# Kernel tuning notes

Hardware: AMD Instinct MI355X
Metric: run time of the kernel (lower is better)

The kernel has to match this reference:

```python
import jax, jax.numpy as jnp
import numpy as np

VOCAB = 32000; PAD = 0
NHID = 512; H = 8; NK = 64; NV = 64; NL = 4
B = 16; S = 511; L = S + 1
N = B * S            # graph nodes after reshape(-1, n_hid)
E = 131072           # edges per graph
EPS = 1e-5
PATTERN = [0, 0, 1, 1, 0, 0, 1, 1]  # n_head==8 -> [gt,gt,attr,attr,gt,gt,attr,attr]


def setup_inputs() -> dict:
    key = jax.random.key(0)
    ks = iter(jax.random.split(key, 48))
    r = lambda *sh: jax.random.normal(next(ks), sh, jnp.float32) * 0.02
    inp = {}
    emb = jax.random.normal(next(ks), (VOCAB, NHID), jnp.float32) * 0.1
    inp['in_embed_w'] = emb.at[PAD].set(0.0)            # padding_idx row is zero
    inp['pos_embed_w'] = jax.random.normal(next(ks), (L, NHID), jnp.float32) * 0.1
    inp['qkv_w'] = r(NL, NHID, H * (2 * NK + NV)); inp['qkv_b'] = r(NL, H * (2 * NK + NV))
    inp['attn_out_w'] = r(NL, H * NV, NHID); inp['attn_out_b'] = r(NL, NHID)
    inp['ff1_w'] = r(NL, NHID, 4 * NHID); inp['ff1_b'] = r(NL, 4 * NHID)
    inp['ff2_w'] = r(NL, 4 * NHID, NHID); inp['ff2_b'] = r(NL, NHID)
    inp['sage1_w'] = r(H, NHID, NHID); inp['sage1_b'] = r(H, NHID)
    inp['sage2_w'] = r(H, NHID, NHID); inp['sage2_b'] = r(H, NHID)
    inp['gc3_w'] = r(H, NHID, NHID // H); inp['gc3_b'] = r(H, NHID // H)
    inp['gcn_ff1_w'] = r(NHID, NHID); inp['gcn_ff1_b'] = r(NHID)
    inp['gcn_ff2_w'] = r(NHID, NHID); inp['gcn_ff2_b'] = r(NHID)
    inp['ln_g'] = jnp.ones((NHID,), jnp.float32)
    inp['ln_b'] = jnp.zeros((NHID,), jnp.float32)
    inp['in_idxs'] = jax.random.randint(next(ks), (B, S), 1, VOCAB)
    inp['mask'] = jnp.ones((B, L, H, L), dtype=bool)
    inp['gt_src'] = jax.random.randint(next(ks), (E,), 0, N)
    inp['gt_dst'] = jax.random.randint(next(ks), (E,), 0, N)
    inp['attr_src'] = jax.random.randint(next(ks), (E,), 0, N)
    inp['attr_dst'] = jax.random.randint(next(ks), (E,), 0, N)
    return inp


def _ln(x, g, b):
    mu = x.mean(-1, keepdims=True)
    v = ((x - mu) ** 2).mean(-1, keepdims=True)
    return (x - mu) / jnp.sqrt(v + EPS) * g + b


def _encode(in_embed_w, pos_embed_w, qkv_w, qkv_b, attn_out_w, attn_out_b,
            ff1_w, ff1_b, ff2_w, ff2_b, sage1_w, sage1_b, sage2_w, sage2_b,
            gc3_w, gc3_b, gcn_ff1_w, gcn_ff1_b, gcn_ff2_w, gcn_ff2_b, ln_g, ln_b,
            in_idxs, mask, gt_src, gt_dst, attr_src, attr_dst):
    # --- embed (pad one pad-token column at the front) ---
    pad_idxs = jnp.pad(in_idxs, ((0, 0), (1, 0)), constant_values=PAD)
    h = in_embed_w[pad_idxs] + pos_embed_w[jnp.arange(L)]        # [B,L,NHID]
    m = mask.transpose(0, 2, 1, 3)                               # [B,H,L,L]
    # --- transformer blocks ---
    for l in range(NL):
        qkv = (h @ qkv_w[l] + qkv_b[l]).reshape(B, L, H, 2 * NK + NV).transpose(0, 2, 1, 3)
        q, k, v = qkv[..., :NK], qkv[..., NK:2 * NK], qkv[..., 2 * NK:]
        sc = jnp.einsum('bhik,bhjk->bhij', q, k) / np.float32(np.sqrt(NK))
        sc = jnp.where(m, sc, -jnp.inf)
        a = jax.nn.softmax(sc, axis=-1)
        o = jnp.einsum('bhij,bhjd->bhid', a, v).transpose(0, 2, 1, 3).reshape(B, L, H * NV)
        attn_ret = h + (o @ attn_out_w[l] + attn_out_b[l])       # attn module returns x + out
        x = h + attn_ret                                         # block adds x again (faithful)
        h = x + (jax.nn.relu(x @ ff1_w[l] + ff1_b[l]) @ ff2_w[l] + ff2_b[l])
    zg, hg = h[:, 0], h[:, 1:]                                   # [B,NHID], [B,S,NHID]
    # --- GCN over flattened nodes ---
    xf = hg.reshape(N, NHID)
    def deg(idx):
        return jax.ops.segment_sum(jnp.ones((E,), jnp.float32), idx, num_segments=N)
    gdata = []
    for src, dst in ((gt_src, gt_dst), (attr_src, attr_dst)):
        gdata.append((src, dst, deg(dst), deg(src)))             # (src, dst, in_deg, out_deg)
    outs = []
    for i in range(H):
        src, dst, ind, outd = gdata[PATTERN[i]]
        def sage(x, W, b):
            # DGL SAGEConv 'gcn': (sum_neigh + self) / (in_deg + 1) then linear
            agg = jax.ops.segment_sum(x[src], dst, num_segments=N)
            return ((agg + x) / (ind + 1.0)[:, None]) @ W + b
        o = sage(xf, sage1_w[i], sage1_b[i])
        o = sage(o, sage2_w[i], sage2_b[i])
        # DGL GraphConv norm='both' (in>out so weight first)
        f = (o @ gc3_w[i]) * (jnp.maximum(outd, 1.0) ** -0.5)[:, None]
        agg = jax.ops.segment_sum(f[src], dst, num_segments=N)
        outs.append(agg * (jnp.maximum(ind, 1.0) ** -0.5)[:, None] + gc3_b[i])
    xc = jnp.concatenate(outs, axis=-1).reshape(B, S, NHID)
    x = hg + _ln(xc, ln_g, ln_b)
    ff = jax.nn.relu(x @ gcn_ff1_w + gcn_ff1_b) @ gcn_ff2_w + gcn_ff2_b
    zbar = x + _ln(ff, ln_g, ln_b)
    return zbar, zg


def reference(in_embed_w, pos_embed_w, qkv_w, qkv_b, attn_out_w, attn_out_b,
              ff1_w, ff1_b, ff2_w, ff2_b, sage1_w, sage1_b, sage2_w, sage2_b,
              gc3_w, gc3_b, gcn_ff1_w, gcn_ff1_b, gcn_ff2_w, gcn_ff2_b, ln_g, ln_b,
              in_idxs, mask, gt_src, gt_dst, attr_src, attr_dst):
    return _encode(in_embed_w, pos_embed_w, qkv_w, qkv_b, attn_out_w, attn_out_b,
                   ff1_w, ff1_b, ff2_w, ff2_b, sage1_w, sage1_b, sage2_w, sage2_b,
                   gc3_w, gc3_b, gcn_ff1_w, gcn_ff1_b, gcn_ff2_w, gcn_ff2_b, ln_g, ln_b,
                   in_idxs, mask, gt_src, gt_dst, attr_src, attr_dst)
```

## Files before the change

### kernel.cpp

```cpp
#include <hip/hip_runtime.h>
#include <hip/hip_bf16.h>

typedef __hip_bfloat16 bf16;
typedef unsigned short u16;
typedef __attribute__((ext_vector_type(8))) short s16x8;
typedef __attribute__((ext_vector_type(4))) float f32x4;

__device__ __forceinline__ float bfb(unsigned short b) {
    union { unsigned u; float f; } v; v.u = ((unsigned)b) << 16; return v.f;
}
__device__ __forceinline__ float ldin(const void* p, size_t i, bool f32) {
    return f32 ? ((const float*)p)[i] : bfb(((const unsigned short*)p)[i]);
}
__device__ __forceinline__ void ld4(const void* p, size_t i, bool f32,
                                    float& x, float& y, float& z, float& w) {
    if (f32) {
        float4 v = *reinterpret_cast<const float4*>((const float*)p + i);
        x = v.x; y = v.y; z = v.z; w = v.w;
    } else {
        ushort4 u = *reinterpret_cast<const ushort4*>((const unsigned short*)p + i);
        x = bfb(u.x); y = bfb(u.y); z = bfb(u.z); w = bfb(u.w);
    }
}
__device__ __forceinline__ u16 f2b(float x) {
    bf16 h = __float2bfloat16(x);
    return *reinterpret_cast<u16*>(&h);
}
__device__ __forceinline__ void split2(float x, u16& h, u16& l) {
    unsigned u = __float_as_uint(x);
    h = (u16)(u >> 16);
    float rem = x - __uint_as_float(u & 0xFFFF0000u);
    l = f2b(rem);
}
__device__ __forceinline__ int xcd_swz(int F, int nwg) {
    return ((nwg & 7) == 0) ? ((F & 7) * (nwg >> 3) + (F >> 3)) : F;
}

constexpr int C_B = 16, C_S = 511, C_L = 512, C_NHID = 512;
constexpr int C_N = C_B * C_S;
constexpr int C_MTOK = C_B * C_L;
constexpr int C_E = 131072;
constexpr int C_QKVD = 1536;

enum : size_t {
    OFF_H     = 0,
    OFF_QKV   = 4194304,
    OFF_O     = 16777216,
    OFF_X     = 20971520,
    OFF_MID   = 25165824,
    OFF_PRE   = 41943040,
    OFF_T8    = OFF_PRE,
    OFF_GCAT0 = OFF_PRE + 262144,
    OFF_GCAT1 = OFF_GCAT0 + 131072,
    OFF_DCAT0 = OFF_GCAT1 + 131072,
    OFF_DCAT1 = OFF_DCAT0 + 256,
    OFF_DEG   = OFF_DCAT1 + 256,
    OFF_FLAG  = OFF_DEG + 32768
};

__global__ void detect_kernel(const unsigned* __restrict__ g, int* __restrict__ flag) {
    *flag = (g[0] == 0x3F800000u) ? 1 : 0;
}

__global__ __launch_bounds__(256) void embed_kernel(
    const void* __restrict__ emb, const void* __restrict__ pos,
    const int* __restrict__ idxs, const int* __restrict__ flag,
    float* __restrict__ h)
{
    const bool f = (*flag) != 0;
    int token = blockIdx.x;
    int tid = threadIdx.x;
    int b = token >> 9, t = token & 511;
    int id = (t == 0) ? 0 : idxs[b * C_S + t - 1];
    size_t eo = (size_t)id * C_NHID, po = (size_t)t * C_NHID, ho = (size_t)token * C_NHID;
    h[ho + tid]       = ldin(emb, eo + tid, f)       + ldin(pos, po + tid, f);
    h[ho + tid + 256] = ldin(emb, eo + tid + 256, f) + ldin(pos, po + tid + 256, f);
}

__global__ __launch_bounds__(256) void wtrans2_kernel(
    const void* __restrict__ Wsrc, size_t srcOff, const int* __restrict__ flag,
    u16* __restrict__ Bh, u16* __restrict__ Bl, int K, int N)
{
    const bool f = (*flag) != 0;
    __shared__ float s[32][33];
    int nb = blockIdx.x << 5, kb = blockIdx.y << 5;
    int c = threadIdx.x & 31, r0 = (threadIdx.x >> 5) << 2;
#pragma unroll
    for (int i = 0; i < 4; ++i)
        s[r0 + i][c] = ldin(Wsrc, srcOff + (size_t)(kb + r0 + i) * N + nb + c, f);
    __syncthreads();
#pragma unroll
    for (int i = 0; i < 4; ++i) {
        u16 h, l;
        split2(s[c][r0 + i], h, l);
        size_t o = (size_t)(nb + r0 + i) * K + kb + c;
        Bh[o] = h; Bl[o] = l;
    }
}

__global__ __launch_bounds__(256, 2) void msgemm_kernel(
    const float* __restrict__ A,
    const u16* __restrict__ Bh, const u16* __restrict__ Bl,
    const void* __restrict__ biasB, size_t bOff,
    const float* __restrict__ biasF,
    const float* __restrict__ res, float resScale,
    const float* __restrict__ rowDeg, int relu,
    const int* __restrict__ flag,
    float* __restrict__ C, int M, int K, int Nc, int ldc)
{
    const bool f32in = (*flag) != 0;
    __shared__ __align__(16) u16 sAh[128][40];
    __shared__ __align__(16) u16 sAl[128][40];
    __shared__ __align__(16) u16 sBh[64][40];
    __shared__ __align__(16) u16 sBl[64][40];
    const int tid = threadIdx.x;
    const int nwg = gridDim.x * gridDim.y;
    const int swz = xcd_swz(blockIdx.y * gridDim.x + blockIdx.x, nwg);
    const int bm = (swz / gridDim.x) << 7, bn = (swz % gridDim.x) << 6;
    const int lane = tid & 63, lr = lane & 15, lg = lane >> 4;
    const int wave = tid >> 6, wm = wave >> 1, wn = wave & 1;

    f32x4 acc[4][2];
#pragma unroll
    for (int m = 0; m < 4; ++m)
#pragma unroll
        for (int n = 0; n < 2; ++n) {
            f32x4 z = {0.f, 0.f, 0.f, 0.f};
            acc[m][n] = z;
        }

    const int sr = tid >> 1, sk = (tid & 1) << 4;
    const int am = bm + sr;
    const bool aok = am < M;
    const float* ap = A + (size_t)am * K + sk;
    const int brn = tid >> 2, bk = (tid & 3) << 3;
    const u16* bph = Bh + (size_t)(bn + brn) * K + bk;
    const u16* bpl = Bl + (size_t)(bn + brn) * K + bk;

    for (int k0 = 0; k0 < K; k0 += 32) {
        u16 tah[16], tal[16];
        if (aok) {
#pragma unroll
            for (int i = 0; i < 16; i += 4) {
                float4 v = *reinterpret_cast<const float4*>(ap + k0 + i);
                split2(v.x, tah[i],     tal[i]);
                split2(v.y, tah[i + 1], tal[i + 1]);
                split2(v.z, tah[i + 2], tal[i + 2]);
                split2(v.w, tah[i + 3], tal[i + 3]);
            }
        } else {
#pragma unroll
            for (int i = 0; i < 16; ++i) { tah[i] = 0; tal[i] = 0; }
        }
        s16x8 bh0 = *reinterpret_cast<const s16x8*>(bph + k0);
        s16x8 bl0 = *reinterpret_cast<const s16x8*>(bpl + k0);

        *reinterpret_cast<s16x8*>(&sAh[sr][sk])     = *reinterpret_cast<s16x8*>(&tah[0]);
        *reinterpret_cast<s16x8*>(&sAh[sr][sk + 8]) = *reinterpret_cast<s16x8*>(&tah[8]);
        *reinterpret_cast<s16x8*>(&sAl[sr][sk])     = *reinterpret_cast<s16x8*>(&tal[0]);
        *reinterpret_cast<s16x8*>(&sAl[sr][sk + 8]) = *reinterpret_cast<s16x8*>(&tal[8]);
        *reinterpret_cast<s16x8*>(&sBh[brn][bk]) = bh0;
        *reinterpret_cast<s16x8*>(&sBl[brn][bk]) = bl0;
        __syncthreads();

        s16x8 fah[4], fal[4], fbh[2], fbl[2];
#pragma unroll
        for (int m = 0; m < 4; ++m) {
            fah[m] = *reinterpret_cast<const s16x8*>(&sAh[wm * 64 + m * 16 + lr][lg * 8]);
            fal[m] = *reinterpret_cast<const s16x8*>(&sAl[wm * 64 + m * 16 + lr][lg * 8]);
        }
#pragma unroll
        for (int n = 0; n < 2; ++n) {
            fbh[n] = *reinterpret_cast<const s16x8*>(&sBh[wn * 32 + n * 16 + lr][lg * 8]);
            fbl[n] = *reinterpret_cast<const s16x8*>(&sBl[wn * 32 + n * 16 + lr][lg * 8]);
        }
#pragma unroll
        for (int m = 0; m < 4; ++m)
#pragma unroll
            for (int n = 0; n < 2; ++n) {
                acc[m][n] = __builtin_amdgcn_mfma_f32_16x16x32_bf16(fah[m], fbh[n], acc[m][n], 0, 0, 0);
                acc[m][n] = __builtin_amdgcn_mfma_f32_16x16x32_bf16(fah[m], fbl[n], acc[m][n], 0, 0, 0);
                acc[m][n] = __builtin_amdgcn_mfma_f32_16x16x32_bf16(fal[m], fbh[n], acc[m][n], 0, 0, 0);
            }
        __syncthreads();
    }

#pragma unroll
    for (int m = 0; m < 4; ++m) {
#pragma unroll
        for (int r = 0; r < 4; ++r) {
            int row = bm + wm * 64 + m * 16 + lg * 4 + r;
            if (row >= M) continue;
            float rs = rowDeg ? rsqrtf(fmaxf(rowDeg[row], 1.f)) : 1.f;
#pragma unroll
            for (int n = 0; n < 2; ++n) {
                int col = bn + wn * 32 + n * 16 + lr;
                float v = acc[m][n][r];
                if (biasB) v += ldin(biasB, bOff + col, f32in);
                if (biasF) v += biasF[col];
                v *= rs;
                if (res) v += resScale * res[(size_t)row * Nc + col];
                if (relu) v = fmaxf(v, 0.f);
                C[(size_t)row * ldc + col] = v;
            }
        }
    }
}

__global__ __launch_bounds__(256, 2) void msgemm2_kernel(
    const float* __restrict__ A,
    const u16* __restrict__ Bh, const u16* __restrict__ Bl,
    const void* __restrict__ biasB, size_t bOff,
    const int relu, const int* __restrict__ flag,
    float* __restrict__ C, int M, int K, int Nc, int ldc)
{
    const bool f32in = (*flag) != 0;
    __shared__ __align__(16) u16 sAh[128][40];
    __shared__ __align__(16) u16 sAl[128][40];
    __shared__ __align__(16) u16 sBh[128][40];
    __shared__ __align__(16) u16 sBl[128][40];
    const int tid = threadIdx.x;
    const int nwg = gridDim.x * gridDim.y;
    const int swz = xcd_swz(blockIdx.y * gridDim.x + blockIdx.x, nwg);
    const int bm = (swz / gridDim.x) << 7, bn = (swz % gridDim.x) << 7;
    const int lane = tid & 63, lr = lane & 15, lg = lane >> 4;
    const int wave = tid >> 6, wm = wave >> 1, wn = wave & 1;

    f32x4 acc[4][4];
#pragma unroll
    for (int m = 0; m < 4; ++m)
#pragma unroll
        for (int n = 0; n < 4; ++n) {
            f32x4 z = {0.f, 0.f, 0.f, 0.f};
            acc[m][n] = z;
        }

    const int sr = tid >> 1, sk = (tid & 1) << 4;
    const int am = bm + sr;
    const bool aok = am < M;
    const float* ap = A + (size_t)am * K + sk;
    const u16* bph = Bh + (size_t)(bn + sr) * K + sk;
    const u16* bpl = Bl + (size_t)(bn + sr) * K + sk;

    for (int k0 = 0; k0 < K; k0 += 32) {
        u16 tah[16], tal[16];
        if (aok) {
#pragma unroll
            for (int i = 0; i < 16; i += 4) {
                float4 v = *reinterpret_cast<const float4*>(ap + k0 + i);
                split2(v.x, tah[i],     tal[i]);
                split2(v.y, tah[i + 1], tal[i + 1]);
                split2(v.z, tah[i + 2], tal[i + 2]);
                split2(v.w, tah[i + 3], tal[i + 3]);
            }
        } else {
#pragma unroll
            for (int i = 0; i < 16; ++i) { tah[i] = 0; tal[i] = 0; }
        }
        s16x8 bh0 = *reinterpret_cast<const s16x8*>(bph + k0);
        s16x8 bh1 = *reinterpret_cast<const s16x8*>(bph + k0 + 8);
        s16x8 bl0 = *reinterpret_cast<const s16x8*>(bpl + k0);
        s16x8 bl1 = *reinterpret_cast<const s16x8*>(bpl + k0 + 8);

        *reinterpret_cast<s16x8*>(&sAh[sr][sk])     = *reinterpret_cast<s16x8*>(&tah[0]);
        *reinterpret_cast<s16x8*>(&sAh[sr][sk + 8]) = *reinterpret_cast<s16x8*>(&tah[8]);
        *reinterpret_cast<s16x8*>(&sAl[sr][sk])     = *reinterpret_cast<s16x8*>(&tal[0]);
        *reinterpret_cast<s16x8*>(&sAl[sr][sk + 8]) = *reinterpret_cast<s16x8*>(&tal[8]);
        *reinterpret_cast<s16x8*>(&sBh[sr][sk])     = bh0;
        *reinterpret_cast<s16x8*>(&sBh[sr][sk + 8]) = bh1;
        *reinterpret_cast<s16x8*>(&sBl[sr][sk])     = bl0;
        *reinterpret_cast<s16x8*>(&sBl[sr][sk + 8]) = bl1;
        __syncthreads();

        s16x8 fah[4], fal[4], fbh[4], fbl[4];
#pragma unroll
        for (int m = 0; m < 4; ++m) {
            fah[m] = *reinterpret_cast<const s16x8*>(&sAh[wm * 64 + m * 16 + lr][lg * 8]);
            fal[m] = *reinterpret_cast<const s16x8*>(&sAl[wm * 64 + m * 16 + lr][lg * 8]);
        }
#pragma unroll
        for (int n = 0; n < 4; ++n) {
            fbh[n] = *reinterpret_cast<const s16x8*>(&sBh[wn * 64 + n * 16 + lr][lg * 8]);
            fbl[n] = *reinterpret_cast<const s16x8*>(&sBl[wn * 64 + n * 16 + lr][lg * 8]);
        }
#pragma unroll
        for (int m = 0; m < 4; ++m)
#pragma unroll
            for (int n = 0; n < 4; ++n) {
                acc[m][n] = __builtin_amdgcn_mfma_f32_16x16x32_bf16(fah[m], fbh[n], acc[m][n], 0, 0, 0);
                acc[m][n] = __builtin_amdgcn_mfma_f32_16x16x32_bf16(fah[m], fbl[n], acc[m][n], 0, 0, 0);
                acc[m][n] = __builtin_amdgcn_mfma_f32_16x16x32_bf16(fal[m], fbh[n], acc[m][n], 0, 0, 0);
            }
        __syncthreads();
    }

#pragma unroll
    for (int m = 0; m < 4; ++m) {
#pragma unroll
        for (int r = 0; r < 4; ++r) {
            int row = bm + wm * 64 + m * 16 + lg * 4 + r;
            if (row >= M) continue;
#pragma unroll
            for (int n = 0; n < 4; ++n) {
                int col = bn + wn * 64 + n * 16 + lr;
                float v = acc[m][n][r];
                if (biasB) v += ldin(biasB, bOff + col, f32in);
                if (relu) v = fmaxf(v, 0.f);
                C[(size_t)row * ldc + col] = v;
            }
        }
    }
}

__global__ __launch_bounds__(256) void mattn_kernel(
    const float* __restrict__ qkv, float* __restrict__ o_out)
{
    __shared__ __align__(16) u16 sKh[64][72], sKl[64][72];
    __shared__ __align__(16) u16 sVh[64][72], sVl[64][72];
    __shared__ __align__(16) u16 sPh[4][16][72], sPl[4][16][72];
    const int blk = xcd_swz(blockIdx.x, gridDim.x);
    const int b = blk >> 6, h = (blk >> 3) & 7, qt = blk & 7;
    const int tid = threadIdx.x;
    const int lane = tid & 63, lr = lane & 15, lg = lane >> 4;
    const int w = tid >> 6;

    s16x8 qh[2], ql[2];
    {
        const float* qp = qkv + (size_t)(b * C_L + qt * 64 + w * 16 + lr) * C_QKVD + h * 192;
#pragma unroll
        for (int c = 0; c < 2; ++c) {
            int d0 = c * 32 + lg * 8;
            u16 th[8], tl[8];
#pragma unroll
            for (int i = 0; i < 8; i += 4) {
                float4 v = *reinterpret_cast<const float4*>(qp + d0 + i);
                split2(v.x * 0.125f, th[i],     tl[i]);
                split2(v.y * 0.125f, th[i + 1], tl[i + 1]);
                split2(v.z * 0.125f, th[i + 2], tl[i + 2]);
                split2(v.w * 0.125f, th[i + 3], tl[i + 3]);
            }
            qh[c] = *reinterpret_cast<s16x8*>(th);
            ql[c] = *reinterpret_cast<s16x8*>(tl);
        }
    }

    f32x4 accO[4];
#pragma unroll
    for (int n = 0; n < 4; ++n) { f32x4 z = {0.f, 0.f, 0.f, 0.f}; accO[n] = z; }
    float m[4] = {-3.0e38f, -3.0e38f, -3.0e38f, -3.0e38f};
    float l[4] = {0.f, 0.f, 0.f, 0.f};

    const float* kvb = qkv + (size_t)b * C_L * C_QKVD + h * 192;
    const int kp = tid >> 2;
    const int d0 = (tid & 3) << 4;

    for (int jt = 0; jt < 8; ++jt) {
        __syncthreads();
        {
            const float* kr = kvb + (size_t)(jt * 64 + kp) * C_QKVD + 64 + d0;
            const float* vr = kr + 64;
#pragma unroll
            for (int i = 0; i < 16; i += 4) {
                float4 kv = *reinterpret_cast<const float4*>(kr + i);
                float4 vv = *reinterpret_cast<const float4*>(vr + i);
                u16 th[4], tl[4];
                split2(kv.x, th[0], tl[0]); split2(kv.y, th[1], tl[1]);
                split2(kv.z, th[2], tl[2]); split2(kv.w, th[3], tl[3]);
                *reinterpret_cast<ushort4*>(&sKh[kp][d0 + i]) = *reinterpret_cast<ushort4*>(th);
                *reinterpret_cast<ushort4*>(&sKl[kp][d0 + i]) = *reinterpret_cast<ushort4*>(tl);
                u16 hh, ll;
                split2(vv.x, hh, ll); sVh[d0 + i][kp]     = hh; sVl[d0 + i][kp]     = ll;
                split2(vv.y, hh, ll); sVh[d0 + i + 1][kp] = hh; sVl[d0 + i + 1][kp] = ll;
                split2(vv.z, hh, ll); sVh[d0 + i + 2][kp] = hh; sVl[d0 + i + 2][kp] = ll;
                split2(vv.w, hh, ll); sVh[d0 + i + 3][kp] = hh; sVl[d0 + i + 3][kp] = ll;
            }
        }
        __syncthreads();

        f32x4 accS[4];
#pragma unroll
        for (int n = 0; n < 4; ++n) { f32x4 z = {0.f, 0.f, 0.f, 0.f}; accS[n] = z; }
#pragma unroll
        for (int n = 0; n < 4; ++n)
#pragma unroll
            for (int c = 0; c < 2; ++c) {
                s16x8 kh = *reinterpret_cast<const s16x8*>(&sKh[n * 16 + lr][c * 32 + lg * 8]);
                s16x8 kl = *reinterpret_cast<const s16x8*>(&sKl[n * 16 + lr][c * 32 + lg * 8]);
                accS[n] = __builtin_amdgcn_mfma_f32_16x16x32_bf16(qh[c], kh, accS[n], 0, 0, 0);
                accS[n] = __builtin_amdgcn_mfma_f32_16x16x32_bf16(qh[c], kl, accS[n], 0, 0, 0);
                accS[n] = __builtin_amdgcn_mfma_f32_16x16x32_bf16(ql[c], kh, accS[n], 0, 0, 0);
            }

#pragma unroll
        for (int r = 0; r < 4; ++r) {
            float mt = fmaxf(fmaxf(accS[0][r], accS[1][r]), fmaxf(accS[2][r], accS[3][r]));
            mt = fmaxf(mt, __shfl_xor(mt, 1));
            mt = fmaxf(mt, __shfl_xor(mt, 2));
            mt = fmaxf(mt, __shfl_xor(mt, 4));
            mt = fmaxf(mt, __shfl_xor(mt, 8));
            float mn = fmaxf(m[r], mt);
            float corr = __expf(m[r] - mn);
            m[r] = mn;
            float ps = 0.f;
#pragma unroll
            for (int n = 0; n < 4; ++n) {
                float p = __expf(accS[n][r] - mn);
                accS[n][r] = p;
                ps += p;
            }
            ps += __shfl_xor(ps, 1);
            ps += __shfl_xor(ps, 2);
            ps += __shfl_xor(ps, 4);
            ps += __shfl_xor(ps, 8);
            l[r] = l[r] * corr + ps;
#pragma unroll
            for (int n2 = 0; n2 < 4; ++n2) accO[n2][r] *= corr;
        }

#pragma unroll
        for (int r = 0; r < 4; ++r)
#pragma unroll
            for (int n = 0; n < 4; ++n) {
                u16 hh, ll;
                split2(accS[n][r], hh, ll);
                sPh[w][lg * 4 + r][n * 16 + lr] = hh;
                sPl[w][lg * 4 + r][n * 16 + lr] = ll;
            }
        __syncthreads();

#pragma unroll
        for (int n2 = 0; n2 < 4; ++n2)
#pragma unroll
            for (int c = 0; c < 2; ++c) {
                s16x8 ph = *reinterpret_cast<const s16x8*>(&sPh[w][lr][c * 32 + lg * 8]);
                s16x8 pl = *reinterpret_cast<const s16x8*>(&sPl[w][lr][c * 32 + lg * 8]);
                s16x8 vh = *reinterpret_cast<const s16x8*>(&sVh[n2 * 16 + lr][c * 32 + lg * 8]);
                s16x8 vl = *reinterpret_cast<const s16x8*>(&sVl[n2 * 16 + lr][c * 32 + lg * 8]);
                accO[n2] = __builtin_amdgcn_mfma_f32_16x16x32_bf16(ph, vh, accO[n2], 0, 0, 0);
                accO[n2] = __builtin_amdgcn_mfma_f32_16x16x32_bf16(ph, vl, accO[n2], 0, 0, 0);
                accO[n2] = __builtin_amdgcn_mfma_f32_16x16x32_bf16(pl, vh, accO[n2], 0, 0, 0);
            }
    }

#pragma unroll
    for (int r = 0; r < 4; ++r) {
        float inv = 1.f / l[r];
        float* op = o_out + (size_t)(b * C_L + qt * 64 + w * 16 + lg * 4 + r) * C_NHID + h * 64;
#pragma unroll
        for (int n2 = 0; n2 < 4; ++n2)
            op[n2 * 16 + lr] = accO[n2][r] * inv;
    }
}

__global__ __launch_bounds__(256) void sgemm64b_kernel(
    const void* __restrict__ A, int aIn, size_t aOff, size_t zA,
    const void* __restrict__ Wt, int wIn, size_t wOff, size_t zW,
    const int* __restrict__ flag,
    float* __restrict__ C, size_t zC, int M, int K, int Nc)
{
    const bool f32in = (*flag) != 0;
    const bool aF32 = aIn ? f32in : true;
    const bool wF32 = wIn ? f32in : true;
    const size_t za = aOff + (size_t)blockIdx.z * zA;
    const size_t zw = wOff + (size_t)blockIdx.z * zW;
    float* Cz = C + (size_t)blockIdx.z * zC;

    __shared__ float sA[16][68];
    __shared__ float sB[16][68];
    const int tid = threadIdx.x;
    const int tx = tid & 15, ty = tid >> 4;
    const int bm = blockIdx.y << 6, bn = blockIdx.x << 6;
    float acc[4][4] = {};
    const int la_r = tid >> 2;
    const int la_c = (tid & 3) << 2;
    const int lb_r = tid >> 4;
    const int lb_c = (tid & 15) << 2;

    for (int k0 = 0; k0 < K; k0 += 16) {
        float a0, a1, a2, a3, b0, b1, b2, b3;
        ld4(A, za + (size_t)(bm + la_r) * K + k0 + la_c, aF32, a0, a1, a2, a3);
        ld4(Wt, zw + (size_t)(k0 + lb_r) * Nc + bn + lb_c, wF32, b0, b1, b2, b3);
        sA[la_c + 0][la_r] = a0; sA[la_c + 1][la_r] = a1;
        sA[la_c + 2][la_r] = a2; sA[la_c + 3][la_r] = a3;
        sB[lb_r][lb_c + 0] = b0; sB[lb_r][lb_c + 1] = b1;
        sB[lb_r][lb_c + 2] = b2; sB[lb_r][lb_c + 3] = b3;
        __syncthreads();
#pragma unroll
        for (int kk = 0; kk < 16; ++kk) {
            float av[4], bv[4];
#pragma unroll
            for (int i = 0; i < 4; ++i) av[i] = sA[kk][(ty << 2) + i];
#pragma unroll
            for (int j = 0; j < 4; ++j) bv[j] = sB[kk][(tx << 2) + j];
#pragma unroll
            for (int i = 0; i < 4; ++i)
#pragma unroll
                for (int j = 0; j < 4; ++j)
                    acc[i][j] += av[i] * bv[j];
        }
        __syncthreads();
    }
#pragma unroll
    for (int i = 0; i < 4; ++i)
#pragma unroll
        for (int j = 0; j < 4; ++j)
            Cz[(size_t)(bm + (ty << 2) + i) * Nc + bn + (tx << 2) + j] = acc[i][j];
}

__global__ __launch_bounds__(256) void gcatT2_kernel(
    const float* __restrict__ Gtmp,
    u16* __restrict__ G0h, u16* __restrict__ G0l,
    u16* __restrict__ G1h, u16* __restrict__ G1l)
{
    int idx = blockIdx.x * 256 + threadIdx.x;
    int i = idx >> 15, rem = idx & 32767;
    int k = rem >> 6, c = rem & 63;
    int g = (i >> 1) & 1;
    int slot = (i & 1) + ((i >> 2) << 1);
    u16 h, l;
    split2(Gtmp[idx], h, l);
    size_t o = (size_t)(slot * 64 + c) * 512 + k;
    if (g) { G1h[o] = h; G1l[o] = l; }
    else   { G0h[o] = h; G0l[o] = l; }
}

__global__ __launch_bounds__(256) void xfcopy_kernel(
    const float* __restrict__ h, float* __restrict__ xf)
{
    int idx = blockIdx.x * 256 + threadIdx.x;
    int n = idx >> 9, c = idx & 511;
    int b = n / C_S;
    int s = n - b * C_S;
    xf[idx] = h[(((size_t)(b * C_L + 1 + s)) << 9) + c];
}

__global__ __launch_bounds__(256) void degi_kernel(
    const int* __restrict__ gs, const int* __restrict__ gd,
    const int* __restrict__ as_, const int* __restrict__ ad,
    int* __restrict__ ideg0, int* __restrict__ ideg1,
    float* __restrict__ outd0, float* __restrict__ outd1)
{
    int e = blockIdx.x * 256 + threadIdx.x;
    if (e >= C_E) return;
    atomicAdd(&ideg0[gd[e]], 1);
    atomicAdd(&ideg1[ad[e]], 1);
    atomicAdd(&outd0[gs[e]], 1.f);
    atomicAdd(&outd1[as_[e]], 1.f);
}

__global__ __launch_bounds__(1024) void scan_kernel(
    const int* __restrict__ i0, const int* __restrict__ i1,
    int* __restrict__ r0, int* __restrict__ r1)
{
    __shared__ int part[1024];
    const int t = threadIdx.x;
    const int* d = blockIdx.x ? i1 : i0;
    int* rs = blockIdx.x ? r1 : r0;
    int v[8]; int s = 0;
#pragma unroll
    for (int i = 0; i < 8; ++i) {
        int idx = t * 8 + i;
        v[i] = (idx < C_N) ? d[idx] : 0;
        s += v[i];
    }
    part[t] = s;
    __syncthreads();
    for (int off = 1; off < 1024; off <<= 1) {
        int x = (t >= off) ? part[t - off] : 0;
        __syncthreads();
        part[t] += x;
        __syncthreads();
    }
    int run = part[t] - s;
#pragma unroll
    for (int i = 0; i < 8; ++i) {
        int idx = t * 8 + i;
        if (idx <= C_N) rs[idx] = run;
        run += v[i];
    }
}

__global__ __launch_bounds__(256) void fill_kernel(
    const int* __restrict__ gs, const int* __restrict__ gd,
    const int* __restrict__ as_, const int* __restrict__ ad,
    const int* __restrict__ rs0, const int* __restrict__ rs1,
    int* __restrict__ cur0, int* __restrict__ cur1,
    int* __restrict__ csr0, int* __restrict__ csr1)
{
    int e = blockIdx.x * 256 + threadIdx.x;
    if (e >= C_E) return;
    int d0 = gd[e];
    int p = atomicAdd(&cur0[d0], 1);
    csr0[rs0[d0] + p] = gs[e];
    int d1 = ad[e];
    int q = atomicAdd(&cur1[d1], 1);
    csr1[rs1[d1] + q] = as_[e];
}

__global__ __launch_bounds__(256) void gatherA_kernel(
    const float* __restrict__ X, const int* __restrict__ csr,
    const int* __restrict__ rs, float* __restrict__ Y)
{
    const int n = blockIdx.x;
    const int tid = threadIdx.x;
    const int s0 = rs[n], s1 = rs[n + 1];
    const size_t o = (size_t)n * 512;
    float a0 = X[o + tid], a1 = X[o + tid + 256];
    for (int e = s0; e < s1; ++e) {
        const size_t so = (size_t)csr[e] * 512;
        a0 += X[so + tid];
        a1 += X[so + tid + 256];
    }
    const float r = 1.f / (float)(s1 - s0 + 1);
    Y[o + tid] = a0 * r;
    Y[o + tid + 256] = a1 * r;
}

__global__ __launch_bounds__(256) void gatherF_kernel(
    const float* __restrict__ F, const int* __restrict__ csr,
    const int* __restrict__ rs, float* __restrict__ xcagg,
    int c0, int c1, int c2, int c3)
{
    const int n = blockIdx.x;
    const int c = threadIdx.x;
    const int s0 = rs[n], s1 = rs[n + 1];
    float acc = 0.f;
    for (int e = s0; e < s1; ++e)
        acc += F[(size_t)csr[e] * 256 + c];
    const int s = c >> 6, cc = c & 63;
    const int cmap = (s == 0) ? c0 : (s == 1) ? c1 : (s == 2) ? c2 : c3;
    xcagg[(size_t)n * 512 + cmap + cc] = acc;
}

__global__ __launch_bounds__(256) void fxc_kernel(
    float* __restrict__ xcagg, const int* __restrict__ rs0,
    const int* __restrict__ rs1, const void* __restrict__ g3b,
    const int* __restrict__ flag)
{
    const bool f = (*flag) != 0;
    unsigned idx = blockIdx.x * 256 + threadIdx.x;
    int n = idx >> 7;
    int c = (idx & 127) << 2;
    int hh = c >> 6;
    int g = (hh >> 1) & 1;
    const int* rs = g ? rs1 : rs0;
    float ind = (float)(rs[n + 1] - rs[n]);
    float r = rsqrtf(fmaxf(ind, 1.f));
    size_t o = (size_t)n * 512 + c;
    float4 v = *reinterpret_cast<float4*>(xcagg + o);
    v.x = v.x * r + ldin(g3b, c, f);     v.y = v.y * r + ldin(g3b, c + 1, f);
    v.z = v.z * r + ldin(g3b, c + 2, f); v.w = v.w * r + ldin(g3b, c + 3, f);
    *reinterpret_cast<float4*>(xcagg + o) = v;
}

__global__ __launch_bounds__(512) void dvec_kernel(
    const void* __restrict__ s1b, const void* __restrict__ s2b,
    const void* __restrict__ g3w, const float* __restrict__ T8,
    const int* __restrict__ flag, float* __restrict__ dc0, float* __restrict__ dc1)
{
    const bool f = (*flag) != 0;
    const int i = blockIdx.x;
    const int c = threadIdx.x & 63;
    const int kg = threadIdx.x >> 6;
    const float* T = T8 + (size_t)i * 32768;
    float acc = 0.f;
    const int kbeg = kg * 64, kend = kbeg + 64;
    for (int k = kbeg; k < kend; ++k)
        acc += ldin(s1b, (size_t)i * 512 + k, f) * T[k * 64 + c]
             + ldin(s2b, (size_t)i * 512 + k, f) * ldin(g3w, (size_t)i * 32768 + (size_t)k * 64 + c, f);
    __shared__ float red[8][64];
    red[kg][c] = acc;
    __syncthreads();
    if (kg == 0) {
        float v = red[0][c] + red[1][c] + red[2][c] + red[3][c]
                + red[4][c] + red[5][c] + red[6][c] + red[7][c];
        int g = (i >> 1) & 1;
        int slot = (i & 1) + ((i >> 2) << 1);
        (g ? dc1 : dc0)[slot * 64 + c] = v;
    }
}

__global__ __launch_bounds__(256) void ln_kernel(
    const float* __restrict__ in, const float* __restrict__ res,
    const void* __restrict__ gw, const void* __restrict__ bw,
    const int* __restrict__ flag, float* __restrict__ out)
{
    const bool f = (*flag) != 0;
    int row = blockIdx.x;
    int tid = threadIdx.x;
    const float* x = in + (size_t)row * 512;
    float v0 = x[tid], v1 = x[tid + 256];
    __shared__ float red[4];
    float s = v0 + v1;
#pragma unroll
    for (int off = 32; off > 0; off >>= 1) s += __shfl_down(s, off);
    if ((tid & 63) == 0) red[tid >> 6] = s;
    __syncthreads();
    float mu = (red[0] + red[1] + red[2] + red[3]) * (1.f / 512.f);
    __syncthreads();
    float d0 = v0 - mu, d1 = v1 - mu;
    s = d0 * d0 + d1 * d1;
#pragma unroll
    for (int off = 32; off > 0; off >>= 1) s += __shfl_down(s, off);
    if ((tid & 63) == 0) red[tid >> 6] = s;
    __syncthreads();
    float var = (red[0] + red[1] + red[2] + red[3]) * (1.f / 512.f);
    float rstd = rsqrtf(var + 1e-5f);
    size_t o = (size_t)row * 512;
    float r0 = d0 * rstd * ldin(gw, tid, f)       + ldin(bw, tid, f);
    float r1 = d1 * rstd * ldin(gw, tid + 256, f) + ldin(bw, tid + 256, f);
    if (res) { r0 += res[o + tid]; r1 += res[o + tid + 256]; }
    out[o + tid] = r0;
    out[o + tid + 256] = r1;
}

__global__ __launch_bounds__(256) void out_zbar_kernel(
    const float* __restrict__ z, void* __restrict__ out, const int* __restrict__ flag)
{
    const bool f = (*flag) != 0;
    int idx = blockIdx.x * 256 + threadIdx.x;
    if (f) ((float*)out)[idx] = z[idx];
    else   ((bf16*)out)[idx]  = __float2bfloat16(z[idx]);
}

__global__ __launch_bounds__(256) void out_zg_kernel(
    const float* __restrict__ h, void* __restrict__ out, const int* __restrict__ flag)
{
    const bool f = (*flag) != 0;
    int idx = blockIdx.x * 256 + threadIdx.x;
    int b = idx >> 9, c = idx & 511;
    float v = h[(size_t)b * C_L * 512 + c];
    size_t o = (size_t)C_N * 512 + idx;
    if (f) ((float*)out)[o] = v;
    else   ((bf16*)out)[o]  = __float2bfloat16(v);
}

static inline void msgemm(hipStream_t st,
    const float* A, const u16* Bh, const u16* Bl,
    const void* biasB, size_t bOff, const float* biasF,
    const float* res, float resScale, const float* rowDeg, int relu,
    const int* flag, float* C, int M, int K, int Nc, int ldc)
{
    dim3 g(Nc / 64, (M + 127) / 128);
    msgemm_kernel<<<g, dim3(256), 0, st>>>(A, Bh, Bl, biasB, bOff, biasF,
                                           res, resScale, rowDeg, relu, flag,
                                           C, M, K, Nc, ldc);
}

static inline void msgemm2(hipStream_t st,
    const float* A, const u16* Bh, const u16* Bl,
    const void* biasB, size_t bOff, int relu,
    const int* flag, float* C, int M, int K, int Nc, int ldc)
{
    dim3 g(Nc / 128, (M + 127) / 128);
    msgemm2_kernel<<<g, dim3(256), 0, st>>>(A, Bh, Bl, biasB, bOff, relu, flag,
                                            C, M, K, Nc, ldc);
}

static inline void wtrans2(hipStream_t st, const void* Wsrc, size_t srcOff,
                           const int* flag, u16* Bh, u16* Bl, int K, int N)
{
    wtrans2_kernel<<<dim3(N / 32, K / 32), dim3(256), 0, st>>>(
        Wsrc, srcOff, flag, Bh, Bl, K, N);
}

extern "C" void kernel_launch(void* const* d_in, const int* in_sizes, int n_in,
                              void* d_out, int out_size, void* d_ws, size_t ws_size,
                              hipStream_t stream)
{
    const void* emb   = d_in[0];
    const void* pos   = d_in[1];
    const void* qkv_w = d_in[2];
    const void* qkv_b = d_in[3];
    const void* aow   = d_in[4];
    const void* aob   = d_in[5];
    const void* ff1w  = d_in[6];
    const void* ff1b  = d_in[7];
    const void* ff2w  = d_in[8];
    const void* ff2b  = d_in[9];
    const void* s1w   = d_in[10];
    const void* s1b   = d_in[11];
    const void* s2w   = d_in[12];
    const void* s2b   = d_in[13];
    const void* g3w   = d_in[14];
    const void* g3b   = d_in[15];
    const void* gf1w  = d_in[16];
    const void* gf1b  = d_in[17];
    const void* gf2w  = d_in[18];
    const void* gf2b  = d_in[19];
    const void* lng   = d_in[20];
    const void* lnb   = d_in[21];
    const int* idxs   = (const int*)d_in[22];
    const int* gts    = (const int*)d_in[24];
    const int* gtd    = (const int*)d_in[25];
    const int* ats    = (const int*)d_in[26];
    const int* atd    = (const int*)d_in[27];

    float* W = (float*)d_ws;
    float* h    = W + OFF_H;
    float* qkvb = W + OFF_QKV;
    float* ob   = W + OFF_O;
    float* xb   = W + OFF_X;
    float* midb = W + OFF_MID;
    int* flag   = (int*)(W + OFF_FLAG);

    detect_kernel<<<dim3(1), dim3(1), 0, stream>>>((const unsigned*)lng, flag);

    embed_kernel<<<dim3(C_MTOK), dim3(256), 0, stream>>>(emb, pos, idxs, flag, h);

    u16* qkvT = (u16*)ob;
    u16* aoT  = (u16*)midb;
    u16* ffT  = (u16*)qkvb;

    for (int l = 0; l < 4; ++l) {
        wtrans2(stream, qkv_w, (size_t)l * 512 * 1536, flag,
                qkvT, qkvT + 786432, 512, 1536);
        msgemm2(stream, h, qkvT, qkvT + 786432, qkv_b, (size_t)l * 1536,
                0, flag, qkvb, C_MTOK, 512, 1536, 1536);
        mattn_kernel<<<dim3(1024), dim3(256), 0, stream>>>(qkvb, ob);
        wtrans2(stream, aow, (size_t)l * 512 * 512, flag,
                aoT, aoT + 262144, 512, 512);
        msgemm(stream, ob, aoT, aoT + 262144, aob, (size_t)l * 512, nullptr,
               h, 2.f, nullptr, 0, flag, xb, C_MTOK, 512, 512, 512);
        wtrans2(stream, ff1w, (size_t)l * 512 * 2048, flag,
                ffT, ffT + 1048576, 512, 2048);
        msgemm2(stream, xb, ffT, ffT + 1048576, ff1b, (size_t)l * 2048,
                1, flag, midb, C_MTOK, 512, 2048, 2048);
        wtrans2(stream, ff2w, (size_t)l * 2048 * 512, flag,
                ffT + 2097152, ffT + 3145728, 2048, 512);
        msgemm(stream, midb, ffT + 2097152, ffT + 3145728, ff2b, (size_t)l * 512, nullptr,
               xb, 1.f, nullptr, 0, flag, h, C_MTOK, 2048, 512, 512);
    }

    float* xf    = ob;
    float* Z0    = qkvb;
    float* Z1    = qkvb + 4194304;
    float* Yb    = qkvb + 8388608;
    float* Gtmp  = Yb;
    float* Fb    = xb;
    float* zbar  = xb;
    float* xcagg = midb;
    float* xgnn  = midb + 4194304;
    float* fmid  = midb + 8388608;
    float* fout  = midb + 12582912;
    float* T8    = W + OFF_T8;
    float* dc0   = W + OFF_DCAT0;
    float* dc1   = W + OFF_DCAT1;
    float* outd0 = W + OFF_DEG;
    float* outd1 = outd0 + 8192;
    u16* GcT0h = (u16*)(W + OFF_GCAT0);
    u16* GcT0l = GcT0h + 131072;
    u16* GcT1h = (u16*)(W + OFF_GCAT1);
    u16* GcT1l = GcT1h + 131072;
    u16* gfT   = (u16*)Yb;

    int* ibase = (int*)fmid;
    int* rs0   = ibase;
    int* rs1   = ibase + 8208;
    int* ideg0 = ibase + 16416;
    int* ideg1 = ibase + 24608;
    int* cur0  = ibase + 32800;
    int* cur1  = ibase + 40992;
    int* csr0  = ibase + 49184;
    int* csr1  = ibase + 180256;

    xfcopy_kernel<<<dim3(C_N * 512 / 256), dim3(256), 0, stream>>>(h, xf);

    (void)hipMemsetAsync(ideg0, 0, 2 * 8192 * sizeof(int), stream);
    (void)hipMemsetAsync(cur0, 0, 2 * 8192 * sizeof(int), stream);
    (void)hipMemsetAsync(outd0, 0, 2 * 8192 * sizeof(float), stream);
    degi_kernel<<<dim3(C_E / 256), dim3(256), 0, stream>>>(
        gts, gtd, ats, atd, ideg0, ideg1, outd0, outd1);
    scan_kernel<<<dim3(2), dim3(1024), 0, stream>>>(ideg0, ideg1, rs0, rs1);
    fill_kernel<<<dim3(C_E / 256), dim3(256), 0, stream>>>(
        gts, gtd, ats, atd, rs0, rs1, cur0, cur1, csr0, csr1);

    sgemm64b_kernel<<<dim3(1, 8, 8), dim3(256), 0, stream>>>(
        s2w, 1, 0, 262144, g3w, 1, 0, 32768, flag, T8, 32768, 512, 512, 64);
    sgemm64b_kernel<<<dim3(1, 8, 8), dim3(256), 0, stream>>>(
        s1w, 1, 0, 262144, T8, 0, 0, 32768, flag, Gtmp, 32768, 512, 512, 64);
    gcatT2_kernel<<<dim3(1024), dim3(256), 0, stream>>>(Gtmp, GcT0h, GcT0l, GcT1h, GcT1l);
    dvec_kernel<<<dim3(8), dim3(512), 0, stream>>>(s1b, s2b, g3w, T8, flag, dc0, dc1);

    gatherA_kernel<<<dim3(C_N), dim3(256), 0, stream>>>(xf, csr0, rs0, Yb);
    gatherA_kernel<<<dim3(C_N), dim3(256), 0, stream>>>(Yb, csr0, rs0, Z0);
    gatherA_kernel<<<dim3(C_N), dim3(256), 0, stream>>>(xf, csr1, rs1, Yb);
    gatherA_kernel<<<dim3(C_N), dim3(256), 0, stream>>>(Yb, csr1, rs1, Z1);

    msgemm(stream, Z0, GcT0h, GcT0l, nullptr, 0, dc0, nullptr, 0.f, outd0, 0, flag,
           Fb, C_N, 512, 256, 256);
    gatherF_kernel<<<dim3(C_N), dim3(256), 0, stream>>>(
        Fb, csr0, rs0, xcagg, 0, 64, 256, 320);
    msgemm(stream, Z1, GcT1h, GcT1l, nullptr, 0, dc1, nullptr, 0.f, outd1, 0, flag,
           Fb, C_N, 512, 256, 256);
    gatherF_kernel<<<dim3(C_N), dim3(256), 0, stream>>>(
        Fb, csr1, rs1, xcagg, 128, 192, 384, 448);
    fxc_kernel<<<dim3(C_N * 128 / 256), dim3(256), 0, stream>>>(
        xcagg, rs0, rs1, g3b, flag);

    ln_kernel<<<dim3(C_N), dim3(256), 0, stream>>>(xcagg, xf, lng, lnb, flag, xgnn);
    wtrans2(stream, gf1w, 0, flag, gfT, gfT + 262144, 512, 512);
    msgemm(stream, xgnn, gfT, gfT + 262144, gf1b, 0, nullptr,
           nullptr, 0.f, nullptr, 1, flag, fmid, C_N, 512, 512, 512);
    wtrans2(stream, gf2w, 0, flag, gfT + 524288, gfT + 786432, 512, 512);
    msgemm(stream, fmid, gfT + 524288, gfT + 786432, gf2b, 0, nullptr,
           nullptr, 0.f, nullptr, 0, flag, fout, C_N, 512, 512, 512);
    ln_kernel<<<dim3(C_N), dim3(256), 0, stream>>>(fout, xgnn, lng, lnb, flag, zbar);

    out_zbar_kernel<<<dim3(C_N * 512 / 256), dim3(256), 0, stream>>>(zbar, d_out, flag);
    out_zg_kernel<<<dim3(32), dim3(256), 0, stream>>>(h, d_out, flag);
}
```

Baseline: 2.170 ms.

## Double-buffer LDS tiles and prefetch global loads in split-bf16 GEMM kernels

Both split-precision GEMM kernels now use two LDS buffers and a register prefetch. The next tile is loaded from global memory into registers while MFMA work runs on the current tile, and the main loop has one barrier per k-step instead of two. The LDS row padding goes from 40 to 36 u16, and fragment loads and stores are split into 8-byte halves to suit the new stride. This is meant to hide global load latency, at the cost of more LDS and register pressure, which may reduce occupancy under the 2-blocks-per-SM launch bound.

```diff
diff --git a/kernel.cpp b/kernel.cpp
--- a/kernel.cpp
+++ b/kernel.cpp
@@ -4,6 +4,7 @@
 typedef __hip_bfloat16 bf16;
 typedef unsigned short u16;
 typedef __attribute__((ext_vector_type(8))) short s16x8;
+typedef __attribute__((ext_vector_type(4))) short s16x4;
 typedef __attribute__((ext_vector_type(4))) float f32x4;
 
 __device__ __forceinline__ float bfb(unsigned short b) {
@@ -34,6 +35,22 @@
 }
 __device__ __forceinline__ int xcd_swz(int F, int nwg) {
     return ((nwg & 7) == 0) ? ((F & 7) * (nwg >> 3) + (F >> 3)) : F;
+}
+union F8 { s16x8 v; s16x4 h[2]; };
+__device__ __forceinline__ s16x8 ldfrag(const u16* p) {
+    F8 f;
+    f.h[0] = *reinterpret_cast<const s16x4*>(p);
+    f.h[1] = *reinterpret_cast<const s16x4*>(p + 4);
+    return f.v;
+}
+__device__ __forceinline__ void stfrag(u16* p, s16x8 v) {
+    F8 f; f.v = v;
+    *reinterpret_cast<s16x4*>(p)     = f.h[0];
+    *reinterpret_cast<s16x4*>(p + 4) = f.h[1];
+}
+__device__ __forceinline__ void barsync() {
+    asm volatile("s_waitcnt lgkmcnt(0)" ::: "memory");
+    __builtin_amdgcn_s_barrier();
 }
 
 constexpr int C_B = 16, C_S = 511, C_L = 512, C_NHID = 512;
@@ -109,10 +126,10 @@
     float* __restrict__ C, int M, int K, int Nc, int ldc)
 {
     const bool f32in = (*flag) != 0;
-    __shared__ __align__(16) u16 sAh[128][40];
-    __shared__ __align__(16) u16 sAl[128][40];
-    __shared__ __align__(16) u16 sBh[64][40];
-    __shared__ __align__(16) u16 sBl[64][40];
+    __shared__ __align__(16) u16 sAh[2][128][36];
+    __shared__ __align__(16) u16 sAl[2][128][36];
+    __shared__ __align__(16) u16 sBh[2][64][36];
+    __shared__ __align__(16) u16 sBl[2][64][36];
     const int tid = threadIdx.x;
     const int nwg = gridDim.x * gridDim.y;
     const int swz = xcd_swz(blockIdx.y * gridDim.x + blockIdx.x, nwg);
@@ -137,42 +154,63 @@
     const u16* bph = Bh + (size_t)(bn + brn) * K + bk;
     const u16* bpl = Bl + (size_t)(bn + brn) * K + bk;
 
-    for (int k0 = 0; k0 < K; k0 += 32) {
+    float4 a0, a1, a2, a3;
+    s16x8 pbh, pbl;
+
+    auto ld_tile = [&](int kk) {
+        if (aok) {
+            a0 = *reinterpret_cast<const float4*>(ap + kk);
+            a1 = *reinterpret_cast<const float4*>(ap + kk + 4);
+            a2 = *reinterpret_cast<const float4*>(ap + kk + 8);
+            a3 = *reinterpret_cast<const float4*>(ap + kk + 12);
+        }
+        pbh = *reinterpret_cast<const s16x8*>(bph + kk);
+        pbl = *reinterpret_cast<const s16x8*>(bpl + kk);
+    };
+    auto st_tile = [&](int buf) {
         u16 tah[16], tal[16];
         if (aok) {
-#pragma unroll
-            for (int i = 0; i < 16; i += 4) {
-                float4 v = *reinterpret_cast<const float4*>(ap + k0 + i);
-                split2(v.x, tah[i],     tal[i]);
-                split2(v.y, tah[i + 1], tal[i + 1]);
-                split2(v.z, tah[i + 2], tal[i + 2]);
-                split2(v.w, tah[i + 3], tal[i + 3]);
-            }
+            split2(a0.x, tah[0], tal[0]);  split2(a0.y, tah[1], tal[1]);
+            split2(a0.z, tah[2], tal[2]);  split2(a0.w, tah[3], tal[3]);
+            split2(a1.x, tah[4], tal[4]);  split2(a1.y, tah[5], tal[5]);
+            split2(a1.z, tah[6], tal[6]);  split2(a1.w, tah[7], tal[7]);
+            split2(a2.x, tah[8], tal[8]);  split2(a2.y, tah[9], tal[9]);
+            split2(a2.z, tah[10], tal[10]); split2(a2.w, tah[11], tal[11]);
+            split2(a3.x, tah[12], tal[12]); split2(a3.y, tah[13], tal[13]);
+            split2(a3.z, tah[14], tal[14]); split2(a3.w, tah[15], tal[15]);
         } else {
 #pragma unroll
             for (int i = 0; i < 16; ++i) { tah[i] = 0; tal[i] = 0; }
         }
-        s16x8 bh0 = *reinterpret_cast<const s16x8*>(bph + k0);
-        s16x8 bl0 = *reinterpret_cast<const s16x8*>(bpl + k0);
-
-        *reinterpret_cast<s16x8*>(&sAh[sr][sk])     = *reinterpret_cast<s16x8*>(&tah[0]);
-        *reinterpret_cast<s16x8*>(&sAh[sr][sk + 8]) = *reinterpret_cast<s16x8*>(&tah[8]);
-        *reinterpret_cast<s16x8*>(&sAl[sr][sk])     = *reinterpret_cast<s16x8*>(&tal[0]);
-        *reinterpret_cast<s16x8*>(&sAl[sr][sk + 8]) = *reinterpret_cast<s16x8*>(&tal[8]);
-        *reinterpret_cast<s16x8*>(&sBh[brn][bk]) = bh0;
-        *reinterpret_cast<s16x8*>(&sBl[brn][bk]) = bl0;
-        __syncthreads();
-
+        stfrag(&sAh[buf][sr][sk],     *reinterpret_cast<s16x8*>(&tah[0]));
+        stfrag(&sAh[buf][sr][sk + 8], *reinterpret_cast<s16x8*>(&tah[8]));
+        stfrag(&sAl[buf][sr][sk],     *reinterpret_cast<s16x8*>(&tal[0]));
+        stfrag(&sAl[buf][sr][sk + 8], *reinterpret_cast<s16x8*>(&tal[8]));
+        stfrag(&sBh[buf][brn][bk], pbh);
+        stfrag(&sBl[buf][brn][bk], pbl);
+    };
+
+    ld_tile(0);
+    st_tile(0);
+    ld_tile((32 < K) ? 32 : 0);
+    barsync();
+
+    int cur = 0;
+    for (int k0 = 0; k0 < K; k0 += 32) {
+        if (k0 + 32 < K) {
+            st_tile(cur ^ 1);
+            ld_tile((k0 + 64 < K) ? k0 + 64 : 0);
+        }
         s16x8 fah[4], fal[4], fbh[2], fbl[2];
 #pragma unroll
         for (int m = 0; m < 4; ++m) {
-            fah[m] = *reinterpret_cast<const s16x8*>(&sAh[wm * 64 + m * 16 + lr][lg * 8]);
-            fal[m] = *reinterpret_cast<const s16x8*>(&sAl[wm * 64 + m * 16 + lr][lg * 8]);
+            fah[m] = ldfrag(&sAh[cur][wm * 64 + m * 16 + lr][lg * 8]);
+            fal[m] = ldfrag(&sAl[cur][wm * 64 + m * 16 + lr][lg * 8]);
         }
 #pragma unroll
         for (int n = 0; n < 2; ++n) {
-            fbh[n] = *reinterpret_cast<const s16x8*>(&sBh[wn * 32 + n * 16 + lr][lg * 8]);
-            fbl[n] = *reinterpret_cast<const s16x8*>(&sBl[wn * 32 + n * 16 + lr][lg * 8]);
+            fbh[n] = ldfrag(&sBh[cur][wn * 32 + n * 16 + lr][lg * 8]);
+            fbl[n] = ldfrag(&sBl[cur][wn * 32 + n * 16 + lr][lg * 8]);
         }
 #pragma unroll
         for (int m = 0; m < 4; ++m)
@@ -182,7 +220,8 @@
                 acc[m][n] = __builtin_amdgcn_mfma_f32_16x16x32_bf16(fah[m], fbl[n], acc[m][n], 0, 0, 0);
                 acc[m][n] = __builtin_amdgcn_mfma_f32_16x16x32_bf16(fal[m], fbh[n], acc[m][n], 0, 0, 0);
             }
-        __syncthreads();
+        barsync();
+        cur ^= 1;
     }
 
 #pragma unroll
@@ -215,10 +254,10 @@
     float* __restrict__ C, int M, int K, int Nc, int ldc)
 {
     const bool f32in = (*flag) != 0;
-    __shared__ __align__(16) u16 sAh[128][40];
-    __shared__ __align__(16) u16 sAl[128][40];
-    __shared__ __align__(16) u16 sBh[128][40];
-    __shared__ __align__(16) u16 sBl[128][40];
+    __shared__ __align__(16) u16 sAh[2][128][36];
+    __shared__ __align__(16) u16 sAl[2][128][36];
+    __shared__ __align__(16) u16 sBh[2][128][36];
+    __shared__ __align__(16) u16 sBl[2][128][36];
     const int tid = threadIdx.x;
     const int nwg = gridDim.x * gridDim.y;
     const int swz = xcd_swz(blockIdx.y * gridDim.x + blockIdx.x, nwg);
@@ -242,46 +281,67 @@
     const u16* bph = Bh + (size_t)(bn + sr) * K + sk;
     const u16* bpl = Bl + (size_t)(bn + sr) * K + sk;
 
-    for (int k0 = 0; k0 < K; k0 += 32) {
+    float4 a0, a1, a2, a3;
+    s16x8 pbh0, pbh1, pbl0, pbl1;
+
+    auto ld_tile = [&](int kk) {
+        if (aok) {
+            a0 = *reinterpret_cast<const float4*>(ap + kk);
+            a1 = *reinterpret_cast<const float4*>(ap + kk + 4);
+            a2 = *reinterpret_cast<const float4*>(ap + kk + 8);
+            a3 = *reinterpret_cast<const float4*>(ap + kk + 12);
+        }
+        pbh0 = *reinterpret_cast<const s16x8*>(bph + kk);
+        pbh1 = *reinterpret_cast<const s16x8*>(bph + kk + 8);
+        pbl0 = *reinterpret_cast<const s16x8*>(bpl + kk);
+        pbl1 = *reinterpret_cast<const s16x8*>(bpl + kk + 8);
+    };
+    auto st_tile = [&](int buf) {
         u16 tah[16], tal[16];
         if (aok) {
-#pragma unroll
-            for (int i = 0; i < 16; i += 4) {
-                float4 v = *reinterpret_cast<const float4*>(ap + k0 + i);
-                split2(v.x, tah[i],     tal[i]);
-                split2(v.y, tah[i + 1], tal[i + 1]);
-                split2(v.z, tah[i + 2], tal[i + 2]);
-                split2(v.w, tah[i + 3], tal[i + 3]);
-            }
+            split2(a0.x, tah[0], tal[0]);  split2(a0.y, tah[1], tal[1]);
+            split2(a0.z, tah[2], tal[2]);  split2(a0.w, tah[3], tal[3]);
+            split2(a1.x, tah[4], tal[4]);  split2(a1.y, tah[5], tal[5]);
+            split2(a1.z, tah[6], tal[6]);  split2(a1.w, tah[7], tal[7]);
+            split2(a2.x, tah[8], tal[8]);  split2(a2.y, tah[9], tal[9]);
+            split2(a2.z, tah[10], tal[10]); split2(a2.w, tah[11], tal[11]);
+            split2(a3.x, tah[12], tal[12]); split2(a3.y, tah[13], tal[13]);
+            split2(a3.z, tah[14], tal[14]); split2(a3.w, tah[15], tal[15]);
         } else {
 #pragma unroll
             for (int i = 0; i < 16; ++i) { tah[i] = 0; tal[i] = 0; }
         }
-        s16x8 bh0 = *reinterpret_cast<const s16x8*>(bph + k0);
-        s16x8 bh1 = *reinterpret_cast<const s16x8*>(bph + k0 + 8);
-        s16x8 bl0 = *reinterpret_cast<const s16x8*>(bpl + k0);
-        s16x8 bl1 = *reinterpret_cast<const s16x8*>(bpl + k0 + 8);
-
-        *reinterpret_cast<s16x8*>(&sAh[sr][sk])     = *reinterpret_cast<s16x8*>(&tah[0]);
-        *reinterpret_cast<s16x8*>(&sAh[sr][sk + 8]) = *reinterpret_cast<s16x8*>(&tah[8]);
-        *reinterpret_cast<s16x8*>(&sAl[sr][sk])     = *reinterpret_cast<s16x8*>(&tal[0]);
-        *reinterpret_cast<s16x8*>(&sAl[sr][sk + 8]) = *reinterpret_cast<s16x8*>(&tal[8]);
-        *reinterpret_cast<s16x8*>(&sBh[sr][sk])     = bh0;
-        *reinterpret_cast<s16x8*>(&sBh[sr][sk + 8]) = bh1;
-        *reinterpret_cast<s16x8*>(&sBl[sr][sk])     = bl0;
-        *reinterpret_cast<s16x8*>(&sBl[sr][sk + 8]) = bl1;
-        __syncthreads();
-
+        stfrag(&sAh[buf][sr][sk],     *reinterpret_cast<s16x8*>(&tah[0]));
+        stfrag(&sAh[buf][sr][sk + 8], *reinterpret_cast<s16x8*>(&tah[8]));
+        stfrag(&sAl[buf][sr][sk],     *reinterpret_cast<s16x8*>(&tal[0]));
+        stfrag(&sAl[buf][sr][sk + 8], *reinterpret_cast<s16x8*>(&tal[8]));
+        stfrag(&sBh[buf][sr][sk],     pbh0);
+        stfrag(&sBh[buf][sr][sk + 8], pbh1);
+        stfrag(&sBl[buf][sr][sk],     pbl0);
+        stfrag(&sBl[buf][sr][sk + 8], pbl1);
+    };
+
+    ld_tile(0);
+    st_tile(0);
+    ld_tile((32 < K) ? 32 : 0);
+    barsync();
+
+    int cur = 0;
+    for (int k0 = 0; k0 < K; k0 += 32) {
+        if (k0 + 32 < K) {
+            st_tile(cur ^ 1);
+            ld_tile((k0 + 64 < K) ? k0 + 64 : 0);
+        }
         s16x8 fah[4], fal[4], fbh[4], fbl[4];
 #pragma unroll
         for (int m = 0; m < 4; ++m) {
-            fah[m] = *reinterpret_cast<const s16x8*>(&sAh[wm * 64 + m * 16 + lr][lg * 8]);
-            fal[m] = *reinterpret_cast<const s16x8*>(&sAl[wm * 64 + m * 16 + lr][lg * 8]);
+            fah[m] = ldfrag(&sAh[cur][wm * 64 + m * 16 + lr][lg * 8]);
+            fal[m] = ldfrag(&sAl[cur][wm * 64 + m * 16 + lr][lg * 8]);
         }
 #pragma unroll
         for (int n = 0; n < 4; ++n) {
-            fbh[n] = *reinterpret_cast<const s16x8*>(&sBh[wn * 64 + n * 16 + lr][lg * 8]);
-            fbl[n] = *reinterpret_cast<const s16x8*>(&sBl[wn * 64 + n * 16 + lr][lg * 8]);
+            fbh[n] = ldfrag(&sBh[cur][wn * 64 + n * 16 + lr][lg * 8]);
+            fbl[n] = ldfrag(&sBl[cur][wn * 64 + n * 16 + lr][lg * 8]);
         }
 #pragma unroll
         for (int m = 0; m < 4; ++m)
@@ -291,7 +351,8 @@
                 acc[m][n] = __builtin_amdgcn_mfma_f32_16x16x32_bf16(fah[m], fbl[n], acc[m][n], 0, 0, 0);
                 acc[m][n] = __builtin_amdgcn_mfma_f32_16x16x32_bf16(fal[m], fbh[n], acc[m][n], 0, 0, 0);
             }
-        __syncthreads();
+        barsync();
+        cur ^= 1;
     }
 
 #pragma unroll
```

Result: slower. 2.282 ms (+5.2%).
